# Kernel tuning notes

Hardware: AMD Instinct MI355X
Metric: run time of the kernel (lower is better)

## Reference

```python
import jax, jax.numpy as jnp
import numpy as np

N = 100000      # nodes
E = 1600000     # edges (avg degree 16)
F_IN = 64       # graph_input_dim
HID = 64        # gcn_out_dims (constant)
NG = 128        # number of graphs in batch
GF = 32         # global_input_dim
L1, L2, OUT = 256, 128, 1


def _glorot(k, fan_in, fan_out):
    s = 1.0 / np.sqrt(fan_in)
    return jax.random.uniform(k, (fan_in, fan_out), jnp.float32, -s, s)


def setup_inputs() -> dict:
    key = jax.random.key(0)
    ks = jax.random.split(key, 20)
    x = jax.random.normal(ks[0], (N, F_IN), jnp.float32)
    edge_index = jax.random.randint(ks[1], (2, E), 0, N, jnp.int64)
    # every graph gets a contiguous, non-empty slice of nodes (sorted batch ids)
    batch = (jnp.arange(N, dtype=jnp.int64) * NG) // N
    global_features = jax.random.normal(ks[2], (NG, GF), jnp.float32)
    dims = [F_IN, HID, HID, HID]
    inp = {"x": x, "global_features": global_features}
    for i in range(3):
        inp[f"conv_w{i+1}"] = _glorot(ks[3 + i], dims[i], dims[i + 1])
        inp[f"conv_b{i+1}"] = jnp.zeros((dims[i + 1],), jnp.float32)
    inp["fc_w1"] = _glorot(ks[8], HID * 2 + GF, L1)
    inp["fc_b1"] = jnp.zeros((L1,), jnp.float32)
    inp["fc_w2"] = _glorot(ks[9], L1, L2)
    inp["fc_b2"] = jnp.zeros((L2,), jnp.float32)
    inp["out_w"] = _glorot(ks[10], L2, OUT)
    inp["out_b"] = jnp.zeros((OUT,), jnp.float32)
    inp["edge_index"] = edge_index
    inp["batch"] = batch
    return inp


def _gcn_conv(x, src, dst, w, b, n):
    """PyG GCNConv: x' = D^-1/2 (A + I) D^-1/2 (x W) + b."""
    h = x @ w  # [n, out]
    loop = jnp.arange(n, dtype=src.dtype)
    s = jnp.concatenate([src, loop])
    d = jnp.concatenate([dst, loop])
    deg = jax.ops.segment_sum(jnp.ones(s.shape, h.dtype), d, num_segments=n)
    dinv = jnp.where(deg > 0, jax.lax.rsqrt(deg), 0.0)
    norm = dinv[s] * dinv[d]  # [E+n]
    out = jax.ops.segment_sum(h[s] * norm[:, None], d, num_segments=n)
    return out + b


def _forward(x, global_features, conv_w1, conv_b1, conv_w2, conv_b2,
             conv_w3, conv_b3, fc_w1, fc_b1, fc_w2, fc_b2, out_w, out_b,
             edge_index, batch):
    src, dst = edge_index[0], edge_index[1]
    n = x.shape[0]
    ng = global_features.shape[0]
    for w, b in ((conv_w1, conv_b1), (conv_w2, conv_b2), (conv_w3, conv_b3)):
        x = jax.nn.leaky_relu(_gcn_conv(x, src, dst, w, b, n))
    counts = jax.ops.segment_sum(jnp.ones((n,), x.dtype), batch, num_segments=ng)
    mean_pool = jax.ops.segment_sum(x, batch, num_segments=ng) / counts[:, None]
    max_pool = jax.ops.segment_max(x, batch, num_segments=ng)
    h = jnp.concatenate([mean_pool, max_pool, global_features], axis=1)
    h = jax.nn.leaky_relu(h @ fc_w1 + fc_b1)
    h = jax.nn.leaky_relu(h @ fc_w2 + fc_b2)
    return h @ out_w + out_b


def reference(x, global_features, conv_w1, conv_b1, conv_w2, conv_b2,
              conv_w3, conv_b3, fc_w1, fc_b1, fc_w2, fc_b2, out_w, out_b,
              edge_index, batch):
    return _forward(x, global_features, conv_w1, conv_b1, conv_w2, conv_b2,
                    conv_w3, conv_b3, fc_w1, fc_b1, fc_w2, fc_b2, out_w, out_b,
                    edge_index, batch)
```

## Files before the change

### kernel.cpp

```cpp
#include <hip/hip_runtime.h>
#include <hip/hip_fp16.h>
#include <stdint.h>

#define LRELU(x) ((x) > 0.0f ? (x) : 0.01f * (x))

struct h4 { __half2 a, b; };
struct h8 { __half2 a, b, c, d; };

typedef _Float16 f16x8 __attribute__((ext_vector_type(8)));
typedef float    f32x4 __attribute__((ext_vector_type(4)));

#define EPB 8192
#define PARTS 16


__global__ __launch_bounds__(256) void hist1_kernel(const int* __restrict__ dst,
                                                    int* __restrict__ bhist,
                                                    int nblk, int E, int nbk) {
    __shared__ int h[512];
    int blk = blockIdx.x, t = threadIdx.x;
    for (int i = t; i < nbk; i += 256) h[i] = 0;
    __syncthreads();
    #pragma unroll
    for (int k = 0; k < EPB / 1024; ++k) {
        int i4 = blk * (EPB / 4) + k * 256 + t;
        int e = i4 * 4;
        if (e + 3 < E) {
            int4 d = ((const int4*)dst)[i4];
            atomicAdd(&h[d.x >> 8], 1);
            atomicAdd(&h[d.y >> 8], 1);
            atomicAdd(&h[d.z >> 8], 1);
            atomicAdd(&h[d.w >> 8], 1);
        } else {
            for (int j = e; j < E; ++j) atomicAdd(&h[dst[j] >> 8], 1);
        }
    }
    __syncthreads();
    for (int i = t; i < nbk; i += 256) bhist[i * nblk + blk] = h[i];
}

__global__ __launch_bounds__(256) void scanb_kernel(int* __restrict__ bhist,
                                                    int* __restrict__ btot, int nblk) {
    __shared__ int s[256];
    __shared__ int carry;
    int b = blockIdx.x, t = threadIdx.x;
    if (t == 0) carry = 0;
    __syncthreads();
    for (int c0 = 0; c0 < nblk; c0 += 256) {
        int idx = c0 + t;
        int v = (idx < nblk) ? bhist[b * nblk + idx] : 0;
        s[t] = v;
        __syncthreads();
        for (int off = 1; off < 256; off <<= 1) {
            int a = (t >= off) ? s[t - off] : 0;
            __syncthreads();
            s[t] += a;
            __syncthreads();
        }
        if (idx < nblk) bhist[b * nblk + idx] = s[t] - v + carry;
        __syncthreads();
        if (t == 255) carry += s[255];
        __syncthreads();
    }
    if (t == 0) btot[b] = carry;
}

__global__ __launch_bounds__(512) void bbase_wprep_kernel(const int* __restrict__ btot,
                                                          int* __restrict__ bbase,
                                                          int nbk, int E,
                                                          const float* __restrict__ w1,
                                                          const float* __restrict__ w2,
                                                          const float* __restrict__ w3,
                                                          _Float16* __restrict__ Bf) {
    if (blockIdx.x == 0) {
        __shared__ int s[512];
        int t = threadIdx.x;
        int v = (t < nbk) ? btot[t] : 0;
        s[t] = v;
        __syncthreads();
        for (int off = 1; off < 512; off <<= 1) {
            int a = (t >= off) ? s[t - off] : 0;
            __syncthreads();
            s[t] += a;
            __syncthreads();
        }
        if (t < nbk) bbase[t] = s[t] - v;
        if (t == 0) bbase[nbk] = E;
    } else {
        int bc = blockIdx.x - 1;
        int tid = threadIdx.x;
        if (tid < 256) {
            int layer = bc >> 1, c = bc & 1;
            const float* W = (layer == 0) ? w1 : ((layer == 1) ? w2 : w3);
            int t = tid >> 6, l = tid & 63;
            _Float16* dstp = Bf + ((size_t)(layer * 8 + c * 4 + t) * 64 + l) * 8;
            int n  = t * 16 + (l & 15);
            int kb = c * 32 + (l >> 4) * 8;
            #pragma unroll
            for (int i = 0; i < 8; ++i) dstp[i] = (_Float16)W[(kb + i) * 64 + n];
        }
    }
}

__global__ __launch_bounds__(256) void place_kernel(const int* __restrict__ src,
                                                    const int* __restrict__ dst,
                                                    const int* __restrict__ bbase,
                                                    const int* __restrict__ bhist,
                                                    unsigned* __restrict__ bedge,
                                                    int nblk, int E, int nbk) {
    __shared__ int cur[512];
    int blk = blockIdx.x, t = threadIdx.x;
    for (int i = t; i < nbk; i += 256) cur[i] = bbase[i] + bhist[i * nblk + blk];
    __syncthreads();
    #pragma unroll
    for (int k = 0; k < EPB / 1024; ++k) {
        int i4 = blk * (EPB / 4) + k * 256 + t;
        int e = i4 * 4;
        if (e + 3 < E) {
            int4 s4 = ((const int4*)src)[i4];
            int4 d4 = ((const int4*)dst)[i4];
            int p0 = atomicAdd(&cur[d4.x >> 8], 1);
            int p1 = atomicAdd(&cur[d4.y >> 8], 1);
            int p2 = atomicAdd(&cur[d4.z >> 8], 1);
            int p3 = atomicAdd(&cur[d4.w >> 8], 1);
            bedge[p0] = ((unsigned)s4.x << 8) | (unsigned)(d4.x & 255);
            bedge[p1] = ((unsigned)s4.y << 8) | (unsigned)(d4.y & 255);
            bedge[p2] = ((unsigned)s4.z << 8) | (unsigned)(d4.z & 255);
            bedge[p3] = ((unsigned)s4.w << 8) | (unsigned)(d4.w & 255);
        } else {
            for (int j = e; j < E; ++j) {
                int d = dst[j];
                int pos = atomicAdd(&cur[d >> 8], 1);
                bedge[pos] = ((unsigned)src[j] << 8) | (unsigned)(d & 255);
            }
        }
    }
}

__global__ __launch_bounds__(256) void csr_kernel(const unsigned* __restrict__ bedge,
                                                  const int* __restrict__ bbase,
                                                  int* __restrict__ row_ptr,
                                                  float* __restrict__ dinv,
                                                  int* __restrict__ csr_src,
                                                  const int* __restrict__ batch,
                                                  int* __restrict__ gstart,
                                                  int N, int E, int nbk, int NG) {
    __shared__ int cnt[256];
    __shared__ int s[256];
    __shared__ int cur[256];
    int b = blockIdx.x, t = threadIdx.x;
    int node0 = b << 8;
    int beg = bbase[b], end = bbase[b + 1];
    cnt[t] = 0;
    __syncthreads();
    for (int i = beg + t; i < end; i += 256) atomicAdd(&cnt[bedge[i] & 255u], 1);
    __syncthreads();
    int c = cnt[t];
    s[t] = c;
    __syncthreads();
    for (int off = 1; off < 256; off <<= 1) {
        int a = (t >= off) ? s[t - off] : 0;
        __syncthreads();
        s[t] += a;
        __syncthreads();
    }
    int rp = beg + s[t] - c;
    int node = node0 + t;
    if (node < N) {
        row_ptr[node] = rp;
        dinv[node] = rsqrtf((float)c + 1.0f);
        int bb = batch[node];
        if (node == 0) {
            gstart[bb] = 0;
            gstart[NG] = N;
        } else if (batch[node - 1] != bb) {
            gstart[bb] = node;
        }
    }
    cur[t] = rp;
    if (b == nbk - 1 && t == 0) row_ptr[N] = E;
    __syncthreads();
    for (int i = beg + t; i < end; i += 256) {
        unsigned u = bedge[i];
        int pos = atomicAdd(&cur[u & 255u], 1);
        csr_src[pos] = (int)(u >> 8);
    }
}


__global__ __launch_bounds__(256) void gemm_mfma_kernel(const float* __restrict__ X,
                                                        const _Float16* __restrict__ Bf,
                                                        const float* __restrict__ dinv,
                                                        __half* __restrict__ H, int N) {
    int w = threadIdx.x >> 6;
    int l = threadIdx.x & 63;
    int col = l & 15;
    int kg  = l >> 4;
    int base = blockIdx.x * 64 + w * 16;
    int nodeA = base + col;
    bool okA = nodeA < N;

    f32x4 acc[4] = {};
    #pragma unroll
    for (int c = 0; c < 2; ++c) {
        int k0 = c * 32 + kg * 8;
        f16x8 a = {};
        if (okA) {
            const float* xp = X + (size_t)nodeA * 64 + k0;
            float4 u = *(const float4*)xp;
            float4 v = *(const float4*)(xp + 4);
            a[0] = (_Float16)u.x; a[1] = (_Float16)u.y;
            a[2] = (_Float16)u.z; a[3] = (_Float16)u.w;
            a[4] = (_Float16)v.x; a[5] = (_Float16)v.y;
            a[6] = (_Float16)v.z; a[7] = (_Float16)v.w;
        }
        #pragma unroll
        for (int t = 0; t < 4; ++t) {
            f16x8 b = *(const f16x8*)(Bf + ((size_t)(c * 4 + t) * 64 + l) * 8);
            acc[t] = __builtin_amdgcn_mfma_f32_16x16x32_f16(a, b, acc[t], 0, 0, 0);
        }
    }
    float dvr[4];
    int rowN[4];
    #pragma unroll
    for (int r = 0; r < 4; ++r) {
        rowN[r] = base + kg * 4 + r;
        dvr[r] = (rowN[r] < N) ? dinv[rowN[r]] : 0.0f;
    }
    #pragma unroll
    for (int t = 0; t < 4; ++t) {
        #pragma unroll
        for (int r = 0; r < 4; ++r) {
            if (rowN[r] < N)
                H[(size_t)rowN[r] * 64 + t * 16 + col] = __float2half(acc[t][r] * dvr[r]);
        }
    }
}

#define ACC8(vv, c0, c1, c2, c3, c4, c5, c6, c7)                                \
    { float2 p;                                                                 \
      p = __half22float2((vv).a); c0 += p.x; c1 += p.y;                         \
      p = __half22float2((vv).b); c2 += p.x; c3 += p.y;                         \
      p = __half22float2((vv).c); c4 += p.x; c5 += p.y;                         \
      p = __half22float2((vv).d); c6 += p.x; c7 += p.y; }

__global__ __launch_bounds__(512) void agg_gemm_kernel(const __half* __restrict__ H,
                                                       const int* __restrict__ rp,
                                                       const int* __restrict__ csrc,
                                                       const float* __restrict__ dinv,
                                                       const float* __restrict__ bias,
                                                       const _Float16* __restrict__ Bf,
                                                       __half* __restrict__ Hout, int N) {
    __shared__ _Float16 ylds[16][72];
    int wv = threadIdx.x >> 6;
    int l  = threadIdx.x & 63;
    int base = blockIdx.x * 16;
    int nA = base + wv * 2;
    int nB = nA + 1;
    bool hasA = nA < N;
    bool hasB = nB < N;
    int slot = l >> 3;
    int fo = (l & 7) << 3;
    float a0=0,a1=0,a2=0,a3=0,a4=0,a5=0,a6=0,a7=0;
    float b0=0,b1=0,b2=0,b3=0,b4=0,b5=0,b6=0,b7=0;
    if (hasA) {
        int endA = rp[nA + 1];
        int eA = rp[nA] + slot;
        int endB = hasB ? rp[nB + 1] : 0;
        int eB = hasB ? (rp[nB] + slot) : 0;
        while (eA + 8 < endA && eB + 8 < endB) {
            int sA0 = csrc[eA], sA1 = csrc[eA + 8];
            int sB0 = csrc[eB], sB1 = csrc[eB + 8];
            h8 vA0 = *(const h8*)&H[(size_t)sA0 * 64 + fo];
            h8 vA1 = *(const h8*)&H[(size_t)sA1 * 64 + fo];
            h8 vB0 = *(const h8*)&H[(size_t)sB0 * 64 + fo];
            h8 vB1 = *(const h8*)&H[(size_t)sB1 * 64 + fo];
            ACC8(vA0, a0,a1,a2,a3,a4,a5,a6,a7);
            ACC8(vA1, a0,a1,a2,a3,a4,a5,a6,a7);
            ACC8(vB0, b0,b1,b2,b3,b4,b5,b6,b7);
            ACC8(vB1, b0,b1,b2,b3,b4,b5,b6,b7);
            eA += 16; eB += 16;
        }
        while (eA + 8 < endA) {
            int s0 = csrc[eA], s1 = csrc[eA + 8];
            h8 v0 = *(const h8*)&H[(size_t)s0 * 64 + fo];
            h8 v1 = *(const h8*)&H[(size_t)s1 * 64 + fo];
            ACC8(v0, a0,a1,a2,a3,a4,a5,a6,a7);
            ACC8(v1, a0,a1,a2,a3,a4,a5,a6,a7);
            eA += 16;
        }
        while (eB + 8 < endB) {
            int s0 = csrc[eB], s1 = csrc[eB + 8];
            h8 v0 = *(const h8*)&H[(size_t)s0 * 64 + fo];
            h8 v1 = *(const h8*)&H[(size_t)s1 * 64 + fo];
            ACC8(v0, b0,b1,b2,b3,b4,b5,b6,b7);
            ACC8(v1, b0,b1,b2,b3,b4,b5,b6,b7);
            eB += 16;
        }
        if (eA < endA) {
            h8 v0 = *(const h8*)&H[(size_t)csrc[eA] * 64 + fo];
            ACC8(v0, a0,a1,a2,a3,a4,a5,a6,a7);
        }
        if (eB < endB) {
            h8 v0 = *(const h8*)&H[(size_t)csrc[eB] * 64 + fo];
            ACC8(v0, b0,b1,b2,b3,b4,b5,b6,b7);
        }
        #pragma unroll
        for (int m = 8; m <= 32; m <<= 1) {
            a0 += __shfl_xor(a0, m); a1 += __shfl_xor(a1, m);
            a2 += __shfl_xor(a2, m); a3 += __shfl_xor(a3, m);
            a4 += __shfl_xor(a4, m); a5 += __shfl_xor(a5, m);
            a6 += __shfl_xor(a6, m); a7 += __shfl_xor(a7, m);
            b0 += __shfl_xor(b0, m); b1 += __shfl_xor(b1, m);
            b2 += __shfl_xor(b2, m); b3 += __shfl_xor(b3, m);
            b4 += __shfl_xor(b4, m); b5 += __shfl_xor(b5, m);
            b6 += __shfl_xor(b6, m); b7 += __shfl_xor(b7, m);
        }
        if (l < 8) {
            float4 bv0 = *(const float4*)&bias[fo];
            float4 bv1 = *(const float4*)&bias[fo + 4];
            {
                h8 hs = *(const h8*)&H[(size_t)nA * 64 + fo];
                float2 s0 = __half22float2(hs.a), s1 = __half22float2(hs.b);
                float2 s2 = __half22float2(hs.c), s3 = __half22float2(hs.d);
                float dv = dinv[nA];
                _Float16* yp = &ylds[wv * 2][fo];
                yp[0] = (_Float16)(LRELU(dv * (a0 + s0.x) + bv0.x));
                yp[1] = (_Float16)(LRELU(dv * (a1 + s0.y) + bv0.y));
                yp[2] = (_Float16)(LRELU(dv * (a2 + s1.x) + bv0.z));
                yp[3] = (_Float16)(LRELU(dv * (a3 + s1.y) + bv0.w));
                yp[4] = (_Float16)(LRELU(dv * (a4 + s2.x) + bv1.x));
                yp[5] = (_Float16)(LRELU(dv * (a5 + s2.y) + bv1.y));
                yp[6] = (_Float16)(LRELU(dv * (a6 + s3.x) + bv1.z));
                yp[7] = (_Float16)(LRELU(dv * (a7 + s3.y) + bv1.w));
            }
            if (hasB) {
                h8 hs = *(const h8*)&H[(size_t)nB * 64 + fo];
                float2 s0 = __half22float2(hs.a), s1 = __half22float2(hs.b);
                float2 s2 = __half22float2(hs.c), s3 = __half22float2(hs.d);
                float dv = dinv[nB];
                _Float16* yp = &ylds[wv * 2 + 1][fo];
                yp[0] = (_Float16)(LRELU(dv * (b0 + s0.x) + bv0.x));
                yp[1] = (_Float16)(LRELU(dv * (b1 + s0.y) + bv0.y));
                yp[2] = (_Float16)(LRELU(dv * (b2 + s1.x) + bv0.z));
                yp[3] = (_Float16)(LRELU(dv * (b3 + s1.y) + bv0.w));
                yp[4] = (_Float16)(LRELU(dv * (b4 + s2.x) + bv1.x));
                yp[5] = (_Float16)(LRELU(dv * (b5 + s2.y) + bv1.y));
                yp[6] = (_Float16)(LRELU(dv * (b6 + s3.x) + bv1.z));
                yp[7] = (_Float16)(LRELU(dv * (b7 + s3.y) + bv1.w));
            }
        }
    }
    __syncthreads();
    if (wv < 4) {
        int col = l & 15;
        int kg  = l >> 4;
        f32x4 acc = {};
        #pragma unroll
        for (int c = 0; c < 2; ++c) {
            f16x8 a = *(const f16x8*)&ylds[col][c * 32 + kg * 8];
            f16x8 b = *(const f16x8*)(Bf + ((size_t)(c * 4 + wv) * 64 + l) * 8);
            acc = __builtin_amdgcn_mfma_f32_16x16x32_f16(a, b, acc, 0, 0, 0);
        }
        #pragma unroll
        for (int r = 0; r < 4; ++r) {
            int row = base + kg * 4 + r;
            if (row < N)
                Hout[(size_t)row * 64 + wv * 16 + col] = __float2half(acc[r] * dinv[row]);
        }
    }
}

__global__ __launch_bounds__(256) void agg_kernel(const __half* __restrict__ H,
                                                  const int* __restrict__ rp,
                                                  const int* __restrict__ csrc,
                                                  const float* __restrict__ dinv,
                                                  const float* __restrict__ bias,
                                                  __half* __restrict__ Y, int N) {
    int w = (blockIdx.x * blockDim.x + threadIdx.x) >> 6;
    int nA = w << 1;
    if (nA >= N) return;
    int nB = nA + 1;
    bool hasB = nB < N;
    int l = threadIdx.x & 63;
    int slot = l >> 3;
    int fo = (l & 7) << 3;
    int endA = rp[nA + 1];
    int eA = rp[nA] + slot;
    int endB = hasB ? rp[nB + 1] : 0;
    int eB = hasB ? (rp[nB] + slot) : 0;
    float a0=0,a1=0,a2=0,a3=0,a4=0,a5=0,a6=0,a7=0;
    float b0=0,b1=0,b2=0,b3=0,b4=0,b5=0,b6=0,b7=0;
    while (eA + 8 < endA && eB + 8 < endB) {
        int sA0 = csrc[eA], sA1 = csrc[eA + 8];
        int sB0 = csrc[eB], sB1 = csrc[eB + 8];
        h8 vA0 = *(const h8*)&H[(size_t)sA0 * 64 + fo];
        h8 vA1 = *(const h8*)&H[(size_t)sA1 * 64 + fo];
        h8 vB0 = *(const h8*)&H[(size_t)sB0 * 64 + fo];
        h8 vB1 = *(const h8*)&H[(size_t)sB1 * 64 + fo];
        ACC8(vA0, a0,a1,a2,a3,a4,a5,a6,a7);
        ACC8(vA1, a0,a1,a2,a3,a4,a5,a6,a7);
        ACC8(vB0, b0,b1,b2,b3,b4,b5,b6,b7);
        ACC8(vB1, b0,b1,b2,b3,b4,b5,b6,b7);
        eA += 16; eB += 16;
    }
    while (eA + 8 < endA) {
        int s0 = csrc[eA], s1 = csrc[eA + 8];
        h8 v0 = *(const h8*)&H[(size_t)s0 * 64 + fo];
        h8 v1 = *(const h8*)&H[(size_t)s1 * 64 + fo];
        ACC8(v0, a0,a1,a2,a3,a4,a5,a6,a7);
        ACC8(v1, a0,a1,a2,a3,a4,a5,a6,a7);
        eA += 16;
    }
    while (eB + 8 < endB) {
        int s0 = csrc[eB], s1 = csrc[eB + 8];
        h8 v0 = *(const h8*)&H[(size_t)s0 * 64 + fo];
        h8 v1 = *(const h8*)&H[(size_t)s1 * 64 + fo];
        ACC8(v0, b0,b1,b2,b3,b4,b5,b6,b7);
        ACC8(v1, b0,b1,b2,b3,b4,b5,b6,b7);
        eB += 16;
    }
    if (eA < endA) {
        h8 v0 = *(const h8*)&H[(size_t)csrc[eA] * 64 + fo];
        ACC8(v0, a0,a1,a2,a3,a4,a5,a6,a7);
    }
    if (eB < endB) {
        h8 v0 = *(const h8*)&H[(size_t)csrc[eB] * 64 + fo];
        ACC8(v0, b0,b1,b2,b3,b4,b5,b6,b7);
    }
    #pragma unroll
    for (int m = 8; m <= 32; m <<= 1) {
        a0 += __shfl_xor(a0, m); a1 += __shfl_xor(a1, m);
        a2 += __shfl_xor(a2, m); a3 += __shfl_xor(a3, m);
        a4 += __shfl_xor(a4, m); a5 += __shfl_xor(a5, m);
        a6 += __shfl_xor(a6, m); a7 += __shfl_xor(a7, m);
        b0 += __shfl_xor(b0, m); b1 += __shfl_xor(b1, m);
        b2 += __shfl_xor(b2, m); b3 += __shfl_xor(b3, m);
        b4 += __shfl_xor(b4, m); b5 += __shfl_xor(b5, m);
        b6 += __shfl_xor(b6, m); b7 += __shfl_xor(b7, m);
    }
    if (l < 8) {
        float4 bv0 = *(const float4*)&bias[fo];
        float4 bv1 = *(const float4*)&bias[fo + 4];
        {
            h8 hs = *(const h8*)&H[(size_t)nA * 64 + fo];
            float2 s0 = __half22float2(hs.a), s1 = __half22float2(hs.b);
            float2 s2 = __half22float2(hs.c), s3 = __half22float2(hs.d);
            float dv = dinv[nA];
            float o0 = LRELU(dv * (a0 + s0.x) + bv0.x);
            float o1 = LRELU(dv * (a1 + s0.y) + bv0.y);
            float o2 = LRELU(dv * (a2 + s1.x) + bv0.z);
            float o3 = LRELU(dv * (a3 + s1.y) + bv0.w);
            float o4 = LRELU(dv * (a4 + s2.x) + bv1.x);
            float o5 = LRELU(dv * (a5 + s2.y) + bv1.y);
            float o6 = LRELU(dv * (a6 + s3.x) + bv1.z);
            float o7 = LRELU(dv * (a7 + s3.y) + bv1.w);
            h8 o;
            o.a = __floats2half2_rn(o0, o1);
            o.b = __floats2half2_rn(o2, o3);
            o.c = __floats2half2_rn(o4, o5);
            o.d = __floats2half2_rn(o6, o7);
            *(h8*)&Y[(size_t)nA * 64 + fo] = o;
        }
        if (hasB) {
            h8 hs = *(const h8*)&H[(size_t)nB * 64 + fo];
            float2 s0 = __half22float2(hs.a), s1 = __half22float2(hs.b);
            float2 s2 = __half22float2(hs.c), s3 = __half22float2(hs.d);
            float dv = dinv[nB];
            float o0 = LRELU(dv * (b0 + s0.x) + bv0.x);
            float o1 = LRELU(dv * (b1 + s0.y) + bv0.y);
            float o2 = LRELU(dv * (b2 + s1.x) + bv0.z);
            float o3 = LRELU(dv * (b3 + s1.y) + bv0.w);
            float o4 = LRELU(dv * (b4 + s2.x) + bv1.x);
            float o5 = LRELU(dv * (b5 + s2.y) + bv1.y);
            float o6 = LRELU(dv * (b6 + s3.x) + bv1.z);
            float o7 = LRELU(dv * (b7 + s3.y) + bv1.w);
            h8 o;
            o.a = __floats2half2_rn(o0, o1);
            o.b = __floats2half2_rn(o2, o3);
            o.c = __floats2half2_rn(o4, o5);
            o.d = __floats2half2_rn(o6, o7);
            *(h8*)&Y[(size_t)nB * 64 + fo] = o;
        }
    }
}


__global__ __launch_bounds__(256) void pool1_kernel(const __half* __restrict__ Y,
                                                    const int* __restrict__ gstart,
                                                    float* __restrict__ pbuf) {
    __shared__ float ssum[8][64];
    __shared__ float smax[8][64];
    int g = blockIdx.x / PARTS;
    int p = blockIdx.x % PARTS;
    int t = threadIdx.x;
    int f2 = (t & 31) * 2;
    int rg = t >> 5;
    int s = gstart[g], epos = gstart[g + 1];
    int len = epos - s;
    int lo = s + (int)((long long)len * p / PARTS);
    int hi = s + (int)((long long)len * (p + 1) / PARTS);
    float sx = 0.f, sy = 0.f, mx = -3.0e38f, my = -3.0e38f;
    for (int r = lo + rg; r < hi; r += 8) {
        __half2 v = *(const __half2*)&Y[(size_t)r * 64 + f2];
        float2 f = __half22float2(v);
        sx += f.x; sy += f.y;
        mx = fmaxf(mx, f.x); my = fmaxf(my, f.y);
    }
    ssum[rg][f2] = sx; ssum[rg][f2 + 1] = sy;
    smax[rg][f2] = mx; smax[rg][f2 + 1] = my;
    __syncthreads();
    if (t < 64) {
        float ts = 0.f, tm = -3.0e38f;
        #pragma unroll
        for (int r = 0; r < 8; ++r) {
            ts += ssum[r][t];
            tm = fmaxf(tm, smax[r][t]);
        }
        float* row = &pbuf[(size_t)(g * PARTS + p) * 128];
        row[t] = ts;
        row[64 + t] = tm;
    }
}

__global__ __launch_bounds__(256) void mlp_kernel(const float* __restrict__ pbuf,
                                                  const int* __restrict__ gstart,
                                                  const float* __restrict__ gfeat,
                                                  const float* __restrict__ w1,
                                                  const float* __restrict__ b1,
                                                  const float* __restrict__ w2,
                                                  const float* __restrict__ b2,
                                                  const float* __restrict__ w3,
                                                  const float* __restrict__ b3,
                                                  float* __restrict__ out, int NG) {
    __shared__ float hl[160];
    __shared__ float h1[256];
    __shared__ float red[128];
    int g = blockIdx.x, t = threadIdx.x;
    if (t < 64) {
        const float* base = &pbuf[(size_t)g * PARTS * 128];
        float ts = 0.f, tm = -3.0e38f;
        #pragma unroll
        for (int p = 0; p < PARTS; ++p) {
            ts += base[p * 128 + t];
            tm = fmaxf(tm, base[p * 128 + 64 + t]);
        }
        float cnt = (float)(gstart[g + 1] - gstart[g]);
        hl[t] = ts / cnt;
        hl[64 + t] = tm;
    } else if (t >= 128 && t < 160) {
        hl[t] = gfeat[g * 32 + (t - 128)];
    }
    __syncthreads();
    float a1 = b1[t];
    for (int k = 0; k < 160; ++k) a1 += hl[k] * w1[k * 256 + t];
    h1[t] = LRELU(a1);
    __syncthreads();
    if (t < 128) {
        float a2 = b2[t];
        for (int k = 0; k < 256; ++k) a2 += h1[k] * w2[k * 128 + t];
        red[t] = LRELU(a2) * w3[t];
    }
    __syncthreads();
    if (t == 0) {
        float a3 = b3[0];
        for (int k = 0; k < 128; ++k) a3 += red[k];
        out[g] = a3;
    }
}


extern "C" void kernel_launch(void* const* d_in, const int* in_sizes, int n_in,
                              void* d_out, int out_size, void* d_ws, size_t ws_size,
                              hipStream_t stream) {
    const float* x      = (const float*)d_in[0];
    const float* gfeat  = (const float*)d_in[1];
    const float* cw1    = (const float*)d_in[2];
    const float* cb1    = (const float*)d_in[3];
    const float* cw2    = (const float*)d_in[4];
    const float* cb2    = (const float*)d_in[5];
    const float* cw3    = (const float*)d_in[6];
    const float* cb3    = (const float*)d_in[7];
    const float* fw1    = (const float*)d_in[8];
    const float* fb1    = (const float*)d_in[9];
    const float* fw2    = (const float*)d_in[10];
    const float* fb2    = (const float*)d_in[11];
    const float* ow     = (const float*)d_in[12];
    const float* ob     = (const float*)d_in[13];
    const int*   eidx   = (const int*)d_in[14];
    const int*   batch  = (const int*)d_in[15];

    const int N    = in_sizes[0] / 64;
    const int E    = in_sizes[14] / 2;
    const int NG   = in_sizes[1] / 32;
    const int NBUK = (N + 255) >> 8;
    const int NBLK = (E + EPB - 1) / EPB;
    const int* src = eidx;
    const int* dst = eidx + E;

    char* wp = (char*)d_ws;
    auto carve = [&](size_t bytes) {
        void* p = (void*)wp;
        wp += (bytes + 255) & ~(size_t)255;
        return p;
    };
    float*     dinv    = (float*)    carve((size_t)N * 4);
    int*       row_ptr = (int*)      carve((size_t)(N + 1) * 4);
    int*       bhist   = (int*)      carve((size_t)NBUK * NBLK * 4);
    int*       btot    = (int*)      carve((size_t)NBUK * 4);
    int*       bbase   = (int*)      carve((size_t)(NBUK + 1) * 4);
    unsigned*  bedge   = (unsigned*) carve((size_t)E * 4);
    int*       csr_src = (int*)      carve((size_t)E * 4);
    __half*    hA      = (__half*)   carve((size_t)N * 64 * 2);
    __half*    hB      = (__half*)   carve((size_t)N * 64 * 2);
    __half*    ybuf    = (__half*)   carve((size_t)N * 64 * 2);
    int*       gstart  = (int*)      carve((size_t)(NG + 1) * 4);
    float*     pbuf    = (float*)    carve((size_t)NG * PARTS * 128 * 4);
    _Float16*  Bf      = (_Float16*) carve((size_t)3 * 4096 * 2);
    float*     outf    = (float*)d_out;

    hist1_kernel<<<NBLK, 256, 0, stream>>>(dst, bhist, NBLK, E, NBUK);
    scanb_kernel<<<NBUK, 256, 0, stream>>>(bhist, btot, NBLK);
    bbase_wprep_kernel<<<7, 512, 0, stream>>>(btot, bbase, NBUK, E, cw1, cw2, cw3, Bf);
    place_kernel<<<NBLK, 256, 0, stream>>>(src, dst, bbase, bhist, bedge, NBLK, E, NBUK);
    csr_kernel<<<NBUK, 256, 0, stream>>>(bedge, bbase, row_ptr, dinv, csr_src,
                                         batch, gstart, N, E, NBUK, NG);

    const int gemmB  = (N + 63) / 64;
    const int fuseB  = (N + 15) / 16;
    const int aggB   = ((N + 1) / 2 + 3) / 4;

    gemm_mfma_kernel<<<gemmB, 256, 0, stream>>>(x, Bf, dinv, hA, N);
    agg_gemm_kernel<<<fuseB, 512, 0, stream>>>(hA, row_ptr, csr_src, dinv, cb1,
                                               Bf + 4096, hB, N);
    agg_gemm_kernel<<<fuseB, 512, 0, stream>>>(hB, row_ptr, csr_src, dinv, cb2,
                                               Bf + 8192, hA, N);
    agg_kernel<<<aggB, 256, 0, stream>>>(hA, row_ptr, csr_src, dinv, cb3, ybuf, N);

    pool1_kernel<<<NG * PARTS, 256, 0, stream>>>(ybuf, gstart, pbuf);
    mlp_kernel<<<NG, 256, 0, stream>>>(pbuf, gstart, gfeat, fw1, fb1, fw2, fb2, ow, ob, outf, NG);
}
```

Measured before the change: 211.8 us.

## Make fused aggregate+GEMM wave-local using shuffles instead of LDS and block barrier

Each wave now aggregates two nodes and feeds their activations directly into a 16x16x32 MFMA through cross-lane shuffles, rather than staging 16 rows in shared memory and syncing the block before four waves do the GEMM. This removes the __syncthreads and LDS round-trip, and it lets every wave proceed independently with 256-thread blocks. In exchange each wave issues 8 MFMAs in which only 2 of the 16 rows are useful, adds shuffle traffic, and writes outputs as scattered 2-byte stores.

New measurement: 218.8 us. 1.03x slower.

```diff
diff --git a/kernel.cpp b/kernel.cpp
--- a/kernel.cpp
+++ b/kernel.cpp
@@ -244,129 +244,138 @@
       p = __half22float2((vv).c); c4 += p.x; c5 += p.y;                         \
       p = __half22float2((vv).d); c6 += p.x; c7 += p.y; }
 
-__global__ __launch_bounds__(512) void agg_gemm_kernel(const __half* __restrict__ H,
+__global__ __launch_bounds__(256) void agg_gemm_kernel(const __half* __restrict__ H,
                                                        const int* __restrict__ rp,
                                                        const int* __restrict__ csrc,
                                                        const float* __restrict__ dinv,
                                                        const float* __restrict__ bias,
                                                        const _Float16* __restrict__ Bf,
                                                        __half* __restrict__ Hout, int N) {
-    __shared__ _Float16 ylds[16][72];
-    int wv = threadIdx.x >> 6;
-    int l  = threadIdx.x & 63;
-    int base = blockIdx.x * 16;
-    int nA = base + wv * 2;
+    int w = (blockIdx.x * blockDim.x + threadIdx.x) >> 6;
+    int nA = w << 1;
+    if (nA >= N) return;
     int nB = nA + 1;
-    bool hasA = nA < N;
     bool hasB = nB < N;
+    int nBs = hasB ? nB : nA;
+    int l = threadIdx.x & 63;
     int slot = l >> 3;
     int fo = (l & 7) << 3;
+    int endA = rp[nA + 1];
+    int eA = rp[nA] + slot;
+    int endB = hasB ? rp[nB + 1] : 0;
+    int eB = hasB ? (rp[nB] + slot) : 0;
     float a0=0,a1=0,a2=0,a3=0,a4=0,a5=0,a6=0,a7=0;
     float b0=0,b1=0,b2=0,b3=0,b4=0,b5=0,b6=0,b7=0;
-    if (hasA) {
-        int endA = rp[nA + 1];
-        int eA = rp[nA] + slot;
-        int endB = hasB ? rp[nB + 1] : 0;
-        int eB = hasB ? (rp[nB] + slot) : 0;
-        while (eA + 8 < endA && eB + 8 < endB) {
-            int sA0 = csrc[eA], sA1 = csrc[eA + 8];
-            int sB0 = csrc[eB], sB1 = csrc[eB + 8];
-            h8 vA0 = *(const h8*)&H[(size_t)sA0 * 64 + fo];
-            h8 vA1 = *(const h8*)&H[(size_t)sA1 * 64 + fo];
-            h8 vB0 = *(const h8*)&H[(size_t)sB0 * 64 + fo];
-            h8 vB1 = *(const h8*)&H[(size_t)sB1 * 64 + fo];
-            ACC8(vA0, a0,a1,a2,a3,a4,a5,a6,a7);
-            ACC8(vA1, a0,a1,a2,a3,a4,a5,a6,a7);
-            ACC8(vB0, b0,b1,b2,b3,b4,b5,b6,b7);
-            ACC8(vB1, b0,b1,b2,b3,b4,b5,b6,b7);
-            eA += 16; eB += 16;
-        }
-        while (eA + 8 < endA) {
-            int s0 = csrc[eA], s1 = csrc[eA + 8];
-            h8 v0 = *(const h8*)&H[(size_t)s0 * 64 + fo];
-            h8 v1 = *(const h8*)&H[(size_t)s1 * 64 + fo];
-            ACC8(v0, a0,a1,a2,a3,a4,a5,a6,a7);
-            ACC8(v1, a0,a1,a2,a3,a4,a5,a6,a7);
-            eA += 16;
-        }
-        while (eB + 8 < endB) {
-            int s0 = csrc[eB], s1 = csrc[eB + 8];
-            h8 v0 = *(const h8*)&H[(size_t)s0 * 64 + fo];
-            h8 v1 = *(const h8*)&H[(size_t)s1 * 64 + fo];
-            ACC8(v0, b0,b1,b2,b3,b4,b5,b6,b7);
-            ACC8(v1, b0,b1,b2,b3,b4,b5,b6,b7);
-            eB += 16;
-        }
-        if (eA < endA) {
-            h8 v0 = *(const h8*)&H[(size_t)csrc[eA] * 64 + fo];
-            ACC8(v0, a0,a1,a2,a3,a4,a5,a6,a7);
-        }
-        if (eB < endB) {
-            h8 v0 = *(const h8*)&H[(size_t)csrc[eB] * 64 + fo];
-            ACC8(v0, b0,b1,b2,b3,b4,b5,b6,b7);
-        }
+    while (eA + 8 < endA && eB + 8 < endB) {
+        int sA0 = csrc[eA], sA1 = csrc[eA + 8];
+        int sB0 = csrc[eB], sB1 = csrc[eB + 8];
+        h8 vA0 = *(const h8*)&H[(size_t)sA0 * 64 + fo];
+        h8 vA1 = *(const h8*)&H[(size_t)sA1 * 64 + fo];
+        h8 vB0 = *(const h8*)&H[(size_t)sB0 * 64 + fo];
+        h8 vB1 = *(const h8*)&H[(size_t)sB1 * 64 + fo];
+        ACC8(vA0, a0,a1,a2,a3,a4,a5,a6,a7);
+        ACC8(vA1, a0,a1,a2,a3,a4,a5,a6,a7);
+        ACC8(vB0, b0,b1,b2,b3,b4,b5,b6,b7);
+        ACC8(vB1, b0,b1,b2,b3,b4,b5,b6,b7);
+        eA += 16; eB += 16;
+    }
+    while (eA + 8 < endA) {
+        int s0 = csrc[eA], s1 = csrc[eA + 8];
+        h8 v0 = *(const h8*)&H[(size_t)s0 * 64 + fo];
+        h8 v1 = *(const h8*)&H[(size_t)s1 * 64 + fo];
+        ACC8(v0, a0,a1,a2,a3,a4,a5,a6,a7);
+        ACC8(v1, a0,a1,a2,a3,a4,a5,a6,a7);
+        eA += 16;
+    }
+    while (eB + 8 < endB) {
+        int s0 = csrc[eB], s1 = csrc[eB + 8];
+        h8 v0 = *(const h8*)&H[(size_t)s0 * 64 + fo];
+        h8 v1 = *(const h8*)&H[(size_t)s1 * 64 + fo];
+        ACC8(v0, b0,b1,b2,b3,b4,b5,b6,b7);
+        ACC8(v1, b0,b1,b2,b3,b4,b5,b6,b7);
+        eB += 16;
+    }
+    if (eA < endA) {
+        h8 v0 = *(const h8*)&H[(size_t)csrc[eA] * 64 + fo];
+        ACC8(v0, a0,a1,a2,a3,a4,a5,a6,a7);
+    }
+    if (eB < endB) {
+        h8 v0 = *(const h8*)&H[(size_t)csrc[eB] * 64 + fo];
+        ACC8(v0, b0,b1,b2,b3,b4,b5,b6,b7);
+    }
+    #pragma unroll
+    for (int m = 8; m <= 32; m <<= 1) {
+        a0 += __shfl_xor(a0, m); a1 += __shfl_xor(a1, m);
+        a2 += __shfl_xor(a2, m); a3 += __shfl_xor(a3, m);
+        a4 += __shfl_xor(a4, m); a5 += __shfl_xor(a5, m);
+        a6 += __shfl_xor(a6, m); a7 += __shfl_xor(a7, m);
+        b0 += __shfl_xor(b0, m); b1 += __shfl_xor(b1, m);
+        b2 += __shfl_xor(b2, m); b3 += __shfl_xor(b3, m);
+        b4 += __shfl_xor(b4, m); b5 += __shfl_xor(b5, m);
+        b6 += __shfl_xor(b6, m); b7 += __shfl_xor(b7, m);
+    }
+    float4 bv0 = *(const float4*)&bias[fo];
+    float4 bv1 = *(const float4*)&bias[fo + 4];
+    int pa[4], pb[4];
+    {
+        h8 hs = *(const h8*)&H[(size_t)nA * 64 + fo];
+        float2 s0 = __half22float2(hs.a), s1 = __half22float2(hs.b);
+        float2 s2 = __half22float2(hs.c), s3 = __half22float2(hs.d);
+        float dv = dinv[nA];
+        __half2 q0 = __floats2half2_rn(LRELU(dv * (a0 + s0.x) + bv0.x),
+                                       LRELU(dv * (a1 + s0.y) + bv0.y));
+        __half2 q1 = __floats2half2_rn(LRELU(dv * (a2 + s1.x) + bv0.z),
+                                       LRELU(dv * (a3 + s1.y) + bv0.w));
+        __half2 q2 = __floats2half2_rn(LRELU(dv * (a4 + s2.x) + bv1.x),
+                                       LRELU(dv * (a5 + s2.y) + bv1.y));
+        __half2 q3 = __floats2half2_rn(LRELU(dv * (a6 + s3.x) + bv1.z),
+                                       LRELU(dv * (a7 + s3.y) + bv1.w));
+        pa[0] = *(int*)&q0; pa[1] = *(int*)&q1; pa[2] = *(int*)&q2; pa[3] = *(int*)&q3;
+    }
+    {
+        h8 hs = *(const h8*)&H[(size_t)nBs * 64 + fo];
+        float2 s0 = __half22float2(hs.a), s1 = __half22float2(hs.b);
+        float2 s2 = __half22float2(hs.c), s3 = __half22float2(hs.d);
+        float dv = dinv[nBs];
+        __half2 q0 = __floats2half2_rn(LRELU(dv * (b0 + s0.x) + bv0.x),
+                                       LRELU(dv * (b1 + s0.y) + bv0.y));
+        __half2 q1 = __floats2half2_rn(LRELU(dv * (b2 + s1.x) + bv0.z),
+                                       LRELU(dv * (b3 + s1.y) + bv0.w));
+        __half2 q2 = __floats2half2_rn(LRELU(dv * (b4 + s2.x) + bv1.x),
+                                       LRELU(dv * (b5 + s2.y) + bv1.y));
+        __half2 q3 = __floats2half2_rn(LRELU(dv * (b6 + s3.x) + bv1.z),
+                                       LRELU(dv * (b7 + s3.y) + bv1.w));
+        pb[0] = *(int*)&q0; pb[1] = *(int*)&q1; pb[2] = *(int*)&q2; pb[3] = *(int*)&q3;
+    }
+    bool rowB = (l & 15) == 1;
+    int oct = l >> 4;
+    f32x4 acc[4] = {};
+    #pragma unroll
+    for (int c = 0; c < 2; ++c) {
+        int so = c * 4 + oct;
+        union { int u[4]; f16x8 v; } af;
         #pragma unroll
-        for (int m = 8; m <= 32; m <<= 1) {
-            a0 += __shfl_xor(a0, m); a1 += __shfl_xor(a1, m);
-            a2 += __shfl_xor(a2, m); a3 += __shfl_xor(a3, m);
-            a4 += __shfl_xor(a4, m); a5 += __shfl_xor(a5, m);
-            a6 += __shfl_xor(a6, m); a7 += __shfl_xor(a7, m);
-            b0 += __shfl_xor(b0, m); b1 += __shfl_xor(b1, m);
-            b2 += __shfl_xor(b2, m); b3 += __shfl_xor(b3, m);
-            b4 += __shfl_xor(b4, m); b5 += __shfl_xor(b5, m);
-            b6 += __shfl_xor(b6, m); b7 += __shfl_xor(b7, m);
-        }
-        if (l < 8) {
-            float4 bv0 = *(const float4*)&bias[fo];
-            float4 bv1 = *(const float4*)&bias[fo + 4];
-            {
-                h8 hs = *(const h8*)&H[(size_t)nA * 64 + fo];
-                float2 s0 = __half22float2(hs.a), s1 = __half22float2(hs.b);
-                float2 s2 = __half22float2(hs.c), s3 = __half22float2(hs.d);
-                float dv = dinv[nA];
-                _Float16* yp = &ylds[wv * 2][fo];
-                yp[0] = (_Float16)(LRELU(dv * (a0 + s0.x) + bv0.x));
-                yp[1] = (_Float16)(LRELU(dv * (a1 + s0.y) + bv0.y));
-                yp[2] = (_Float16)(LRELU(dv * (a2 + s1.x) + bv0.z));
-                yp[3] = (_Float16)(LRELU(dv * (a3 + s1.y) + bv0.w));
-                yp[4] = (_Float16)(LRELU(dv * (a4 + s2.x) + bv1.x));
-                yp[5] = (_Float16)(LRELU(dv * (a5 + s2.y) + bv1.y));
-                yp[6] = (_Float16)(LRELU(dv * (a6 + s3.x) + bv1.z));
-                yp[7] = (_Float16)(LRELU(dv * (a7 + s3.y) + bv1.w));
-            }
-            if (hasB) {
-                h8 hs = *(const h8*)&H[(size_t)nB * 64 + fo];
-                float2 s0 = __half22float2(hs.a), s1 = __half22float2(hs.b);
-                float2 s2 = __half22float2(hs.c), s3 = __half22float2(hs.d);
-                float dv = dinv[nB];
-                _Float16* yp = &ylds[wv * 2 + 1][fo];
-                yp[0] = (_Float16)(LRELU(dv * (b0 + s0.x) + bv0.x));
-                yp[1] = (_Float16)(LRELU(dv * (b1 + s0.y) + bv0.y));
-                yp[2] = (_Float16)(LRELU(dv * (b2 + s1.x) + bv0.z));
-                yp[3] = (_Float16)(LRELU(dv * (b3 + s1.y) + bv0.w));
-                yp[4] = (_Float16)(LRELU(dv * (b4 + s2.x) + bv1.x));
-                yp[5] = (_Float16)(LRELU(dv * (b5 + s2.y) + bv1.y));
-                yp[6] = (_Float16)(LRELU(dv * (b6 + s3.x) + bv1.z));
-                yp[7] = (_Float16)(LRELU(dv * (b7 + s3.y) + bv1.w));
-            }
-        }
-    }
-    __syncthreads();
-    if (wv < 4) {
-        int col = l & 15;
-        int kg  = l >> 4;
-        f32x4 acc = {};
+        for (int j = 0; j < 4; ++j) {
+            int qa = __shfl(pa[j], so);
+            int qb = __shfl(pb[j], so);
+            af.u[j] = rowB ? qb : qa;
+        }
         #pragma unroll
-        for (int c = 0; c < 2; ++c) {
-            f16x8 a = *(const f16x8*)&ylds[col][c * 32 + kg * 8];
-            f16x8 b = *(const f16x8*)(Bf + ((size_t)(c * 4 + wv) * 64 + l) * 8);
-            acc = __builtin_amdgcn_mfma_f32_16x16x32_f16(a, b, acc, 0, 0, 0);
-        }
+        for (int t = 0; t < 4; ++t) {
+            f16x8 b = *(const f16x8*)(Bf + ((size_t)(c * 4 + t) * 64 + l) * 8);
+            acc[t] = __builtin_amdgcn_mfma_f32_16x16x32_f16(af.v, b, acc[t], 0, 0, 0);
+        }
+    }
+    if (l < 16) {
+        float dvA = dinv[nA];
         #pragma unroll
-        for (int r = 0; r < 4; ++r) {
-            int row = base + kg * 4 + r;
-            if (row < N)
-                Hout[(size_t)row * 64 + wv * 16 + col] = __float2half(acc[r] * dinv[row]);
+        for (int t = 0; t < 4; ++t)
+            Hout[(size_t)nA * 64 + t * 16 + l] = __float2half(acc[t][0] * dvA);
+        if (hasB) {
+            float dvB = dinv[nB];
+            #pragma unroll
+            for (int t = 0; t < 4; ++t)
+                Hout[(size_t)nB * 64 + t * 16 + l] = __float2half(acc[t][1] * dvB);
         }
     }
 }
@@ -626,15 +635,14 @@
     csr_kernel<<<NBUK, 256, 0, stream>>>(bedge, bbase, row_ptr, dinv, csr_src,
                                          batch, gstart, N, E, NBUK, NG);
 
-    const int gemmB  = (N + 63) / 64;
-    const int fuseB  = (N + 15) / 16;
-    const int aggB   = ((N + 1) / 2 + 3) / 4;
+    const int gemmB = (N + 63) / 64;
+    const int aggB  = ((N + 1) / 2 + 3) / 4;
 
     gemm_mfma_kernel<<<gemmB, 256, 0, stream>>>(x, Bf, dinv, hA, N);
-    agg_gemm_kernel<<<fuseB, 512, 0, stream>>>(hA, row_ptr, csr_src, dinv, cb1,
-                                               Bf + 4096, hB, N);
-    agg_gemm_kernel<<<fuseB, 512, 0, stream>>>(hB, row_ptr, csr_src, dinv, cb2,
-                                               Bf + 8192, hA, N);
+    agg_gemm_kernel<<<aggB, 256, 0, stream>>>(hA, row_ptr, csr_src, dinv, cb1,
+                                              Bf + 4096, hB, N);
+    agg_gemm_kernel<<<aggB, 256, 0, stream>>>(hB, row_ptr, csr_src, dinv, cb2,
+                                              Bf + 8192, hA, N);
     agg_kernel<<<aggB, 256, 0, stream>>>(hA, row_ptr, csr_src, dinv, cb3, ybuf, N);
 
     pool1_kernel<<<NG * PARTS, 256, 0, stream>>>(ybuf, gstart, pbuf);
```
